# Optimization experiments

Measured on AMD Instinct MI355X. Metric: run time of the kernel, lower is better.

Reference implementation:

```python
import jax, jax.numpy as jnp
import numpy as np

INT4_QMAX = 7.0  # symmetric int4: representable range clipped to [-8, 7]


def simulate_quantize_int4(w):
    # axis_to_reduce=None -> single global scale over the whole kernel
    scale = jnp.max(jnp.abs(w)) / INT4_QMAX
    q = jnp.clip(jnp.round(w / scale), -8.0, 7.0)
    return q * scale


def setup_inputs() -> dict:
    key = jax.random.key(0)
    k_x, k_w, k_bias, k_a, k_b = jax.random.split(key, 5)
    d_in, features, rank = 1024, 1024, 16
    x = jax.random.normal(k_x, (4, 8192, d_in), dtype=jnp.float32)
    kernel = jax.random.normal(k_w, (d_in, features), dtype=jnp.float32)
    bias = jax.random.normal(k_bias, (features,), dtype=jnp.float32)
    a = jax.random.normal(k_a, (d_in, rank), dtype=jnp.float32) * (1.0 / np.sqrt(d_in))
    b = jax.random.normal(k_b, (rank, features), dtype=jnp.float32) * 0.01
    return {"x": x, "kernel": kernel, "bias": bias, "a": a, "b": b}


def reference(x, kernel, bias, a, b):
    # fake-quantized main matmul: y = x @ dequant(quant(W)) + bias
    w = simulate_quantize_int4(kernel)
    y = jnp.einsum('bsd,df->bsf', x, w) + bias
    # LoRA adapter: x @ a @ b (contract small rank dim first)
    lora = jnp.einsum('bsr,rf->bsf', jnp.einsum('bsd,dr->bsr', x, a), b)
    return y + lora
```

## Files before the change

### kernel.cpp

```cpp
#include <hip/hip_runtime.h>
#include <hip/hip_bf16.h>

typedef __bf16 bf16x8 __attribute__((ext_vector_type(8)));
typedef __bf16 bf16x4 __attribute__((ext_vector_type(4)));
typedef float  f32x4  __attribute__((ext_vector_type(4)));

#define K_DIM 1024
#define N_DIM 1024
#define BM 128
#define BN 128
#define BK 64

typedef unsigned int u32;
typedef u32 __attribute__((address_space(1))) u32_g;
typedef u32 __attribute__((address_space(3))) u32_s;

__device__ __forceinline__ void load16_lds(const void* g, void* s) {
    __builtin_amdgcn_global_load_lds((u32_g*)g, (u32_s*)s, 16, 0, 0);
}

__global__ void maxabs_kernel(const float* __restrict__ w, unsigned int* __restrict__ mx, int n4) {
    int i = blockIdx.x * blockDim.x + threadIdx.x;
    int stride = gridDim.x * blockDim.x;
    float m = 0.f;
    for (; i < n4; i += stride) {
        float4 v = ((const float4*)w)[i];
        m = fmaxf(m, fmaxf(fmaxf(fabsf(v.x), fabsf(v.y)), fmaxf(fabsf(v.z), fabsf(v.w))));
    }
#pragma unroll
    for (int off = 32; off > 0; off >>= 1)
        m = fmaxf(m, __shfl_down(m, off, 64));
    if ((threadIdx.x & 63) == 0) atomicMax(mx, __float_as_uint(m));
}

__global__ void build_w_kernel(const float* __restrict__ kern, const float* __restrict__ amat,
                               const float* __restrict__ bmat, const unsigned int* __restrict__ mx,
                               __bf16* __restrict__ wt) {
    int t = blockIdx.x * blockDim.x + threadIdx.x;
    int k = t & (K_DIM - 1);
    int n = t >> 10;
    float scale = __uint_as_float(*mx) * (1.0f / 7.0f);
    float w = kern[k * N_DIM + n];
    float q = rintf(w / scale);
    q = fminf(fmaxf(q, -8.f), 7.f);
    float acc = q * scale;
#pragma unroll
    for (int r = 0; r < 16; ++r)
        acc += amat[k * 16 + r] * bmat[r * N_DIM + n];
    wt[(size_t)n * K_DIM + k] = (__bf16)acc;
}

__global__ void cvt_x_kernel(const float4* __restrict__ x, bf16x4* __restrict__ xb, int n4) {
    int i = blockIdx.x * blockDim.x + threadIdx.x;
    if (i >= n4) return;
    float4 v = x[i];
    bf16x4 o;
    o.x = (__bf16)v.x; o.y = (__bf16)v.y; o.z = (__bf16)v.z; o.w = (__bf16)v.w;
    xb[i] = o;
}

template <int AMODE>
__global__ __launch_bounds__(256, 2)
void gemm_kernel(const void* __restrict__ Ain, const __bf16* __restrict__ wt,
                 const float* __restrict__ bias, float* __restrict__ out) {
    __shared__ __attribute__((aligned(16))) __bf16 As[BM * BK];
    __shared__ __attribute__((aligned(16))) __bf16 Bs[BN * BK];

    const int tid  = threadIdx.x;
    const int lane = tid & 63;
    const int wave = tid >> 6;
    const int wm = (wave >> 1) * 64;
    const int wn = (wave & 1) * 64;
    const int bm0 = blockIdx.y * BM;
    const int bn0 = blockIdx.x * BN;
    const int l15 = lane & 15;
    const int l4  = lane >> 4;

    f32x4 acc[4][4] = {};

    const int srow = lane >> 3;
    const int gch  = (lane & 7) ^ srow;

    for (int k0 = 0; k0 < K_DIM; k0 += BK) {
        __syncthreads();
#pragma unroll
        for (int i = 0; i < 4; ++i) {
            int r = i * 32 + wave * 8;
            const __bf16* g = wt + (size_t)(bn0 + r + srow) * K_DIM + k0 + gch * 8;
            load16_lds(g, &Bs[r * BK]);
        }
        if (AMODE == 0) {
            const __bf16* xb = (const __bf16*)Ain;
#pragma unroll
            for (int i = 0; i < 4; ++i) {
                int r = i * 32 + wave * 8;
                const __bf16* g = xb + (size_t)(bm0 + r + srow) * K_DIM + k0 + gch * 8;
                load16_lds(g, &As[r * BK]);
            }
        } else {
            const float* x = (const float*)Ain;
#pragma unroll
            for (int j = 0; j < 8; ++j) {
                int f  = j * 256 + tid;
                int r  = f >> 4;
                int c4 = f & 15;
                float4 v = *(const float4*)(x + (size_t)(bm0 + r) * K_DIM + k0 + c4 * 4);
                int p = (c4 >> 1) ^ (r & 7);
                bf16x4 o;
                o.x = (__bf16)v.x; o.y = (__bf16)v.y; o.z = (__bf16)v.z; o.w = (__bf16)v.w;
                *(bf16x4*)(&As[r * BK + p * 8 + (c4 & 1) * 4]) = o;
            }
        }
        __syncthreads();

#pragma unroll
        for (int ks = 0; ks < 2; ++ks) {
            bf16x8 af[4], bfr[4];
#pragma unroll
            for (int mt = 0; mt < 4; ++mt) {
                int r = wm + mt * 16 + l15;
                int p = (ks * 4 + l4) ^ (r & 7);
                af[mt] = *(const bf16x8*)(&As[r * BK + p * 8]);
            }
#pragma unroll
            for (int nt = 0; nt < 4; ++nt) {
                int r = wn + nt * 16 + l15;
                int p = (ks * 4 + l4) ^ (r & 7);
                bfr[nt] = *(const bf16x8*)(&Bs[r * BK + p * 8]);
            }
#pragma unroll
            for (int mt = 0; mt < 4; ++mt)
#pragma unroll
                for (int nt = 0; nt < 4; ++nt)
                    acc[mt][nt] = __builtin_amdgcn_mfma_f32_16x16x32_bf16(
                        af[mt], bfr[nt], acc[mt][nt], 0, 0, 0);
        }
    }

#pragma unroll
    for (int nt = 0; nt < 4; ++nt) {
        int n = bn0 + wn + nt * 16 + l15;
        float bv = bias[n];
#pragma unroll
        for (int mt = 0; mt < 4; ++mt) {
            int m = bm0 + wm + mt * 16 + l4 * 4;
            float* op = out + (size_t)m * N_DIM + n;
#pragma unroll
            for (int r = 0; r < 4; ++r)
                op[(size_t)r * N_DIM] = acc[mt][nt][r] + bv;
        }
    }
}

extern "C" void kernel_launch(void* const* d_in, const int* in_sizes, int n_in,
                              void* d_out, int out_size, void* d_ws, size_t ws_size,
                              hipStream_t stream) {
    const float* x    = (const float*)d_in[0];
    const float* kern = (const float*)d_in[1];
    const float* bias = (const float*)d_in[2];
    const float* amat = (const float*)d_in[3];
    const float* bmat = (const float*)d_in[4];
    float* out = (float*)d_out;
    const int M = in_sizes[0] / K_DIM;

    unsigned int* mx = (unsigned int*)d_ws;
    __bf16* wt = (__bf16*)((char*)d_ws + 256);
    const size_t xb_off    = 256 + (size_t)N_DIM * K_DIM * sizeof(__bf16);
    const size_t need_fast = xb_off + (size_t)M * K_DIM * sizeof(__bf16);

    hipMemsetAsync(d_ws, 0, 4, stream);
    maxabs_kernel<<<256, 256, 0, stream>>>(kern, mx, K_DIM * N_DIM / 4);
    build_w_kernel<<<K_DIM * N_DIM / 256, 256, 0, stream>>>(kern, amat, bmat, mx, wt);

    dim3 grid(N_DIM / BN, M / BM);
    if (ws_size >= need_fast) {
        __bf16* xb = (__bf16*)((char*)d_ws + xb_off);
        int n4 = M * K_DIM / 4;
        cvt_x_kernel<<<(n4 + 255) / 256, 256, 0, stream>>>((const float4*)x, (bf16x4*)xb, n4);
        gemm_kernel<0><<<grid, 256, 0, stream>>>(xb, wt, bias, out);
    } else {
        gemm_kernel<1><<<grid, 256, 0, stream>>>(x, wt, bias, out);
    }
}
```

Baseline: 342.9 us.

## Drop memset via two-stage max, widen x convert, swizzle GEMM tile order, raise occupancy

The max-abs reduction now writes per-block maxima that build_w_kernel reduces itself, which removes the memset launch and the global atomics. The x conversion handles 8 elements per thread with 16-byte stores. The GEMM uses a 1D grid with a grouped tile mapping (8 M-tiles by 8 N-tiles) for better L2 reuse of x and W. Launch bounds rise to 4 blocks per CU, which may cause register pressure or spilling with 64 accumulator floats per thread. The grouped mapping assumes M/BM is a multiple of 8.

```diff
diff --git a/kernel.cpp b/kernel.cpp
--- a/kernel.cpp
+++ b/kernel.cpp
@@ -19,7 +19,8 @@
     __builtin_amdgcn_global_load_lds((u32_g*)g, (u32_s*)s, 16, 0, 0);
 }
 
-__global__ void maxabs_kernel(const float* __restrict__ w, unsigned int* __restrict__ mx, int n4) {
+__global__ void maxabs_kernel(const float* __restrict__ w, float* __restrict__ blockmax, int n4) {
+    __shared__ float sm[4];
     int i = blockIdx.x * blockDim.x + threadIdx.x;
     int stride = gridDim.x * blockDim.x;
     float m = 0.f;
@@ -30,16 +31,32 @@
 #pragma unroll
     for (int off = 32; off > 0; off >>= 1)
         m = fmaxf(m, __shfl_down(m, off, 64));
-    if ((threadIdx.x & 63) == 0) atomicMax(mx, __float_as_uint(m));
+    int lane = threadIdx.x & 63, wave = threadIdx.x >> 6;
+    if (lane == 0) sm[wave] = m;
+    __syncthreads();
+    if (threadIdx.x == 0)
+        blockmax[blockIdx.x] = fmaxf(fmaxf(sm[0], sm[1]), fmaxf(sm[2], sm[3]));
 }
 
 __global__ void build_w_kernel(const float* __restrict__ kern, const float* __restrict__ amat,
-                               const float* __restrict__ bmat, const unsigned int* __restrict__ mx,
+                               const float* __restrict__ bmat, const float* __restrict__ blockmax,
                                __bf16* __restrict__ wt) {
+    __shared__ float smax;
+    if (threadIdx.x < 64) {
+        float m = 0.f;
+#pragma unroll
+        for (int j = 0; j < 4; ++j) m = fmaxf(m, blockmax[threadIdx.x + j * 64]);
+#pragma unroll
+        for (int off = 32; off > 0; off >>= 1)
+            m = fmaxf(m, __shfl_down(m, off, 64));
+        if (threadIdx.x == 0) smax = m;
+    }
+    __syncthreads();
+    float scale = smax * (1.0f / 7.0f);
+
     int t = blockIdx.x * blockDim.x + threadIdx.x;
     int k = t & (K_DIM - 1);
     int n = t >> 10;
-    float scale = __uint_as_float(*mx) * (1.0f / 7.0f);
     float w = kern[k * N_DIM + n];
     float q = rintf(w / scale);
     q = fminf(fmaxf(q, -8.f), 7.f);
@@ -50,17 +67,19 @@
     wt[(size_t)n * K_DIM + k] = (__bf16)acc;
 }
 
-__global__ void cvt_x_kernel(const float4* __restrict__ x, bf16x4* __restrict__ xb, int n4) {
+__global__ void cvt_x_kernel(const float4* __restrict__ x, bf16x8* __restrict__ xb, int n8) {
     int i = blockIdx.x * blockDim.x + threadIdx.x;
-    if (i >= n4) return;
-    float4 v = x[i];
-    bf16x4 o;
-    o.x = (__bf16)v.x; o.y = (__bf16)v.y; o.z = (__bf16)v.z; o.w = (__bf16)v.w;
+    if (i >= n8) return;
+    float4 v0 = x[i * 2];
+    float4 v1 = x[i * 2 + 1];
+    bf16x8 o;
+    o[0] = (__bf16)v0.x; o[1] = (__bf16)v0.y; o[2] = (__bf16)v0.z; o[3] = (__bf16)v0.w;
+    o[4] = (__bf16)v1.x; o[5] = (__bf16)v1.y; o[6] = (__bf16)v1.z; o[7] = (__bf16)v1.w;
     xb[i] = o;
 }
 
 template <int AMODE>
-__global__ __launch_bounds__(256, 2)
+__global__ __launch_bounds__(256, 4)
 void gemm_kernel(const void* __restrict__ Ain, const __bf16* __restrict__ wt,
                  const float* __restrict__ bias, float* __restrict__ out) {
     __shared__ __attribute__((aligned(16))) __bf16 As[BM * BK];
@@ -71,8 +90,12 @@
     const int wave = tid >> 6;
     const int wm = (wave >> 1) * 64;
     const int wn = (wave & 1) * 64;
-    const int bm0 = blockIdx.y * BM;
-    const int bn0 = blockIdx.x * BN;
+
+    const int l = blockIdx.x;
+    const int i = l >> 3;
+    const int bn0 = (i & 7) * BN;
+    const int bm0 = (((i >> 3) << 3) | (l & 7)) * BM;
+
     const int l15 = lane & 15;
     const int l4  = lane >> 4;
 
@@ -84,16 +107,16 @@
     for (int k0 = 0; k0 < K_DIM; k0 += BK) {
         __syncthreads();
 #pragma unroll
-        for (int i = 0; i < 4; ++i) {
-            int r = i * 32 + wave * 8;
+        for (int j = 0; j < 4; ++j) {
+            int r = j * 32 + wave * 8;
             const __bf16* g = wt + (size_t)(bn0 + r + srow) * K_DIM + k0 + gch * 8;
             load16_lds(g, &Bs[r * BK]);
         }
         if (AMODE == 0) {
             const __bf16* xb = (const __bf16*)Ain;
 #pragma unroll
-            for (int i = 0; i < 4; ++i) {
-                int r = i * 32 + wave * 8;
+            for (int j = 0; j < 4; ++j) {
+                int r = j * 32 + wave * 8;
                 const __bf16* g = xb + (size_t)(bm0 + r + srow) * K_DIM + k0 + gch * 8;
                 load16_lds(g, &As[r * BK]);
             }
@@ -163,22 +186,21 @@
     float* out = (float*)d_out;
     const int M = in_sizes[0] / K_DIM;
 
-    unsigned int* mx = (unsigned int*)d_ws;
-    __bf16* wt = (__bf16*)((char*)d_ws + 256);
-    const size_t xb_off    = 256 + (size_t)N_DIM * K_DIM * sizeof(__bf16);
+    float* blockmax = (float*)d_ws;
+    __bf16* wt = (__bf16*)((char*)d_ws + 4096);
+    const size_t xb_off    = 4096 + (size_t)N_DIM * K_DIM * sizeof(__bf16);
     const size_t need_fast = xb_off + (size_t)M * K_DIM * sizeof(__bf16);
 
-    hipMemsetAsync(d_ws, 0, 4, stream);
-    maxabs_kernel<<<256, 256, 0, stream>>>(kern, mx, K_DIM * N_DIM / 4);
-    build_w_kernel<<<K_DIM * N_DIM / 256, 256, 0, stream>>>(kern, amat, bmat, mx, wt);
-
-    dim3 grid(N_DIM / BN, M / BM);
+    maxabs_kernel<<<256, 256, 0, stream>>>(kern, blockmax, K_DIM * N_DIM / 4);
+    build_w_kernel<<<K_DIM * N_DIM / 256, 256, 0, stream>>>(kern, amat, bmat, blockmax, wt);
+
+    const int nblocks = (M / BM) * (N_DIM / BN);
     if (ws_size >= need_fast) {
         __bf16* xb = (__bf16*)((char*)d_ws + xb_off);
-        int n4 = M * K_DIM / 4;
-        cvt_x_kernel<<<(n4 + 255) / 256, 256, 0, stream>>>((const float4*)x, (bf16x4*)xb, n4);
-        gemm_kernel<0><<<grid, 256, 0, stream>>>(xb, wt, bias, out);
+        int n8 = M * K_DIM / 8;
+        cvt_x_kernel<<<(n8 + 255) / 256, 256, 0, stream>>>((const float4*)x, (bf16x8*)xb, n8);
+        gemm_kernel<0><<<nblocks, 256, 0, stream>>>(xb, wt, bias, out);
     } else {
-        gemm_kernel<1><<<grid, 256, 0, stream>>>(x, wt, bias, out);
-    }
-}
+        gemm_kernel<1><<<nblocks, 256, 0, stream>>>(x, wt, bias, out);
+    }
+}
```

Measured after the change: 306.0 us. 10.8% less time.
